# Performance work log

Measured on AMD Instinct MI355X. Metric: run time of the kernel, lower is better.

## Reference

```python
import jax, jax.numpy as jnp
import numpy as np
from jax import lax

B, T, Z, H, F = 64, 256, 128, 512, 64
EPS = 1e-3  # keras LayerNormalization default epsilon


def _glorot(key, shape):
    fan_in, fan_out = shape[0], shape[1]
    lim = np.sqrt(6.0 / (fan_in + fan_out)).astype(np.float32)
    return jax.random.uniform(key, shape, jnp.float32, -lim, lim)


def setup_inputs() -> dict:
    key = jax.random.key(0)
    ks = jax.random.split(key, 16)
    inp = {
        "z": jax.random.normal(ks[0], (B, T, Z), jnp.float32),
        "Wp": _glorot(ks[1], (Z, 2 * H)), "bp": jnp.zeros((2 * H,), jnp.float32),
        "Ws": _glorot(ks[2], (Z, H)), "bs": jnp.zeros((H,), jnp.float32),
        "K0": _glorot(ks[3], (2 * H, 4 * H)), "R0": _glorot(ks[4], (H, 4 * H)), "b0": jnp.zeros((4 * H,), jnp.float32),
        "K1": _glorot(ks[5], (H, 4 * H)), "R1": _glorot(ks[6], (H, 4 * H)), "b1": jnp.zeros((4 * H,), jnp.float32),
        "K2": _glorot(ks[7], (H, 4 * H)), "R2": _glorot(ks[8], (H, 4 * H)), "b2": jnp.zeros((4 * H,), jnp.float32),
        "gamma": jnp.ones((H,), jnp.float32), "beta": jnp.zeros((H,), jnp.float32),
        "W1": _glorot(ks[9], (H, H)), "b1d": jnp.zeros((H,), jnp.float32),
        "W2": _glorot(ks[10], (H, F)), "b2d": jnp.zeros((F,), jnp.float32),
    }
    return inp


def _lstm(x, K, R, b):
    # x: [B, T, D]; keras gate order i, f, g(c), o
    xK = jnp.swapaxes(jnp.einsum('btd,dg->btg', x, K) + b, 0, 1)  # [T, B, 4H]
    h0 = jnp.zeros((x.shape[0], H), x.dtype)
    c0 = jnp.zeros((x.shape[0], H), x.dtype)

    def step(carry, xk):
        h, c = carry
        zg = xk + h @ R
        i, f, g, o = jnp.split(zg, 4, axis=-1)
        c = jax.nn.sigmoid(f) * c + jax.nn.sigmoid(i) * jnp.tanh(g)
        h = jax.nn.sigmoid(o) * jnp.tanh(c)
        return (h, c), h

    _, hs = lax.scan(step, (h0, c0), xK)
    return jnp.swapaxes(hs, 0, 1)  # [B, T, H]


def reference(z, Wp, bp, Ws, bs, K0, R0, b0, K1, R1, b1, K2, R2, b2,
              gamma, beta, W1, b1d, W2, b2d):
    x = jnp.einsum('btz,zd->btd', z, Wp) + bp          # dense_proj -> [B,T,2H]
    residual = jnp.einsum('btz,zh->bth', z, Ws) + bs   # skip_proj  -> [B,T,H]
    x = _lstm(x, K0, R0, b0)
    x = _lstm(x, K1, R1, b1)
    x = x + residual  # use_residual, after layer index 1
    x = _lstm(x, K2, R2, b2)
    # training=False: dropout is identity and attention branch is skipped
    mu = jnp.mean(x, axis=-1, keepdims=True)
    var = jnp.mean(jnp.square(x - mu), axis=-1, keepdims=True)
    x = (x - mu) * lax.rsqrt(var + EPS) * gamma + beta
    x = jax.nn.relu(jnp.einsum('bth,hk->btk', x, W1) + b1d)
    x = jnp.tanh(jnp.einsum('bth,hf->btf', x, W2) + b2d)
    return x
```

## Files before the change

kernel.cpp:

```cpp
#include <hip/hip_runtime.h>
#include <hip/hip_fp16.h>
#include <stdint.h>

typedef unsigned short u16;
typedef unsigned int   u32;
typedef unsigned long long u64;
typedef __attribute__((ext_vector_type(8))) short s16x8;
typedef __attribute__((ext_vector_type(8))) _Float16 h16x8;
typedef __attribute__((ext_vector_type(4))) float f32x4;

#define T_LEN 256

__device__ __forceinline__ u16 f2h(float f){ return __half_as_ushort(__float2half(f)); }
__device__ __forceinline__ h16x8 as_h(s16x8 v){ union{s16x8 s; h16x8 h;} u; u.s=v; return u.h; }
__device__ __forceinline__ float sigm(float x){ return 1.f/(1.f + __expf(-x)); }
__device__ __forceinline__ float tanh_f(float x){ return 2.f*sigm(2.f*x) - 1.f; }

__device__ __forceinline__ s16x8 ldh(const u16* p){
  u64 lo = __hip_atomic_load((const u64*)p,       __ATOMIC_RELAXED, __HIP_MEMORY_SCOPE_AGENT);
  u64 hi = __hip_atomic_load((const u64*)(p + 4), __ATOMIC_RELAXED, __HIP_MEMORY_SCOPE_AGENT);
  union { u64 q[2]; s16x8 v; } u;
  u.q[0] = lo; u.q[1] = hi;
  return u.v;
}

__global__ void k_fuse(const float* __restrict__ Wp, const float* __restrict__ K0,
                       const float* __restrict__ Ws, const float* __restrict__ K2,
                       float* __restrict__ Wf0, float* __restrict__ Wf2)
{
  const int c  = blockIdx.x*256 + threadIdx.x;
  const int by = blockIdx.y;
  float acc[8] = {0,0,0,0,0,0,0,0};
  if (by < 16){
    const int r0 = by*8;
    for (int d = 0; d < 1024; ++d){
      float kv = K0[(size_t)d*2048 + c];
      #pragma unroll
      for (int ii = 0; ii < 8; ++ii) acc[ii] = fmaf(Wp[(size_t)(r0+ii)*1024 + d], kv, acc[ii]);
    }
    #pragma unroll
    for (int ii = 0; ii < 8; ++ii) Wf0[(size_t)(r0+ii)*2048 + c] = acc[ii];
  } else {
    const int r0 = (by-16)*8;
    for (int u = 0; u < 512; ++u){
      float kv = K2[(size_t)u*2048 + c];
      #pragma unroll
      for (int ii = 0; ii < 8; ++ii) acc[ii] = fmaf(Ws[(size_t)(r0+ii)*512 + u], kv, acc[ii]);
    }
    #pragma unroll
    for (int ii = 0; ii < 8; ++ii) Wf2[(size_t)(r0+ii)*2048 + c] = acc[ii];
  }
}

__global__ void k_bias(const float* __restrict__ bp, const float* __restrict__ K0,
                       const float* __restrict__ b0, const float* __restrict__ bs,
                       const float* __restrict__ K2, const float* __restrict__ b2,
                       float* __restrict__ gb0, float* __restrict__ gb2)
{
  const int bx = blockIdx.x;
  if (bx < 8){
    int c = bx*256 + threadIdx.x;
    float a = b0[c];
    for (int d = 0; d < 1024; ++d) a = fmaf(bp[d], K0[(size_t)d*2048 + c], a);
    gb0[c] = a;
  } else {
    int c = (bx-8)*256 + threadIdx.x;
    float a = b2[c];
    for (int u = 0; u < 512; ++u) a = fmaf(bs[u], K2[(size_t)u*2048 + c], a);
    gb2[c] = a;
  }
}

__global__ void k_zero(u32* __restrict__ hbz, int* __restrict__ done)
{
  int idx = blockIdx.x*256 + threadIdx.x;
  if (idx < 196608) hbz[idx] = 0u;
  if (blockIdx.x == 0 && threadIdx.x < 3) done[threadIdx.x*32] = 0;
}

__device__ __forceinline__ size_t gidx(int k, int c, int K32c){
  int gate = c >> 9, u = c & 511;
  int jj = u >> 3, uu = u & 7;
  int lc = gate*8 + uu;
  return ((size_t)(jj*2 + (lc>>4))*K32c + (k>>5))*512
         + (size_t)((((k>>3)&3)*16 + (lc&15))*8) + (size_t)(k&7);
}
__device__ __forceinline__ size_t fidx(int k, int c){
  return ((size_t)(c>>4)*16 + (k>>5))*512
         + (size_t)((((k>>3)&3)*16 + (c&15))*8) + (size_t)(k&7);
}

__global__ void k_pack(const float* __restrict__ R0, const float* __restrict__ Wf0,
                       const float* __restrict__ R1, const float* __restrict__ K1,
                       const float* __restrict__ R2, const float* __restrict__ K2,
                       const float* __restrict__ Wf2, const float* __restrict__ W1,
                       const float* __restrict__ W2, const float* __restrict__ z,
                       u16* __restrict__ wgt0, u16* __restrict__ wgt1, u16* __restrict__ wgt2,
                       u16* __restrict__ w1p,  u16* __restrict__ w2p,  u16* __restrict__ zp)
{
  const long NT = 8159232;
  for (long i = (long)blockIdx.x*256 + threadIdx.x; i < NT; i += (long)gridDim.x*256){
    if (i < 1310720){
      int k = (int)(i >> 11), c = (int)(i & 2047);
      float v = (k < 512) ? R0[(size_t)k*2048 + c] : Wf0[(size_t)(k-512)*2048 + c];
      wgt0[gidx(k, c, 20)] = f2h(v);
    } else if (i < 3407872){
      long i2 = i - 1310720; int k = (int)(i2 >> 11), c = (int)(i2 & 2047);
      float v = (k < 512) ? R1[(size_t)k*2048 + c] : K1[(size_t)(k-512)*2048 + c];
      wgt1[gidx(k, c, 32)] = f2h(v);
    } else if (i < 5767168){
      long i2 = i - 3407872; int k = (int)(i2 >> 11), c = (int)(i2 & 2047);
      float v = (k < 512)  ? R2[(size_t)k*2048 + c]
              : (k < 1024) ? K2[(size_t)(k-512)*2048 + c]
                           : Wf2[(size_t)(k-1024)*2048 + c];
      wgt2[gidx(k, c, 36)] = f2h(v);
    } else if (i < 6029312){
      long i2 = i - 5767168; int k = (int)(i2 >> 9), c = (int)(i2 & 511);
      w1p[fidx(k, c)] = f2h(W1[(size_t)k*512 + c]);
    } else if (i < 6062080){
      long i2 = i - 6029312; int k = (int)(i2 >> 6), c = (int)(i2 & 63);
      w2p[fidx(k, c)] = f2h(W2[(size_t)k*64 + c]);
    } else {
      long i2 = i - 6062080;
      int bb = (int)(i2 >> 15), rem = (int)(i2 & 32767);
      int tt = rem >> 7, k = rem & 127;
      zp[(((size_t)tt*4 + (bb>>4))*4 + (k>>5))*512
         + (size_t)((((k>>3)&3)*16 + (bb&15))*8) + (size_t)(k&7)] = f2h(z[i2]);
    }
  }
}

__global__ __launch_bounds__(256, 1) void k_wave(
    const u16* __restrict__ wgt0, const u16* __restrict__ wgt1, const u16* __restrict__ wgt2,
    const u16* __restrict__ zp, u16* __restrict__ hb, float* __restrict__ hout,
    int* done, u64* __restrict__ ackdump, const float* __restrict__ gb0,
    const float* __restrict__ b1g, const float* __restrict__ gb2)
{
  __shared__ __align__(16) u16 wsm[2*36*512];
  __shared__ float zg[64][33];
  __shared__ __align__(16) u16 hsh[64][8];
  const int tid = threadIdx.x;
  const int bid = blockIdx.x;
  const int L   = bid >> 6;
  const int j   = bid & 63;
  const int K32r = (L==0) ? 20 : ((L==1) ? 32 : 36);

  { const u16* wsrc = (L==0) ? wgt0 + (size_t)j*20480
                    : (L==1) ? wgt1 + (size_t)j*32768
                             : wgt2 + (size_t)j*36864;
    const uint4* s4 = (const uint4*)wsrc; uint4* d4 = (uint4*)wsm;
    const int n4 = K32r*128;
    for (int i = tid; i < n4; i += 256) d4[i] = s4[i]; }

  const int b    = tid & 63;
  const int q    = tid >> 6;
  const int w    = q;
  const int lane = tid & 63;

  float bias[2][4];
  { const float* bsrc = (L==0) ? gb0 : (L==1) ? b1g : gb2;
    #pragma unroll
    for (int ci = 0; ci < 2; ++ci){
      int ucol = j*8 + 2*q + ci;
      #pragma unroll
      for (int g = 0; g < 4; ++g) bias[ci][g] = bsrc[g*512 + ucol];
    } }
  float cst0 = 0.f, cst1 = 0.f;
  u64 ackacc = 0;

  const int smt   = tid >> 5;
  const int sbm   = (tid >> 1) & 15;
  const int shalf = tid & 1;
  const size_t schunk = ((size_t)(smt*16 + (j>>2))*64 + ((j&3)*16 + sbm))*8 + shalf*4;

  __syncthreads();

  for (int s = 0; s < T_LEN + 2; ++s){
    if (tid == 0){
      int g = 0;
      for (;;){
        int okk = 1;
        if (L > 0)
          okk &= (__hip_atomic_load(&done[(L-1)*32], __ATOMIC_RELAXED, __HIP_MEMORY_SCOPE_AGENT) >= 64*s);
        okk &= (__hip_atomic_load(&done[L*32],     __ATOMIC_RELAXED, __HIP_MEMORY_SCOPE_AGENT) >= 64*s);
        if (L < 2)
          okk &= (__hip_atomic_load(&done[(L+1)*32], __ATOMIC_RELAXED, __HIP_MEMORY_SCOPE_AGENT) >= 64*(s-2));
        if (okk || ++g > (1<<20)) break;
        __builtin_amdgcn_s_sleep(8);
      }
    }
    __syncthreads();

    const int t = s - L;
    float hv0 = 0.f, hv1 = 0.f;
    if (t >= 0 && t < T_LEN){
      const int slp = (s + 3) & 3;
      f32x4 acc0 = {0.f,0.f,0.f,0.f};
      f32x4 acc1 = {0.f,0.f,0.f,0.f};
      const size_t wl8 = (size_t)w*8192 + (size_t)lane*8;
      const u16* h0p = hb + (size_t)(0*4 + slp)*32768 + wl8;
      const u16* h1p = hb + (size_t)(1*4 + slp)*32768 + wl8;
      const u16* h2p = hb + (size_t)(2*4 + slp)*32768 + wl8;
      const u16* zpt = zp + (size_t)t*8192 + (size_t)w*2048 + (size_t)lane*8;

      if (L == 0){
        s16x8 areg[20];
        #pragma unroll
        for (int kk = 0; kk < 16; ++kk) areg[kk] = ldh(h0p + (size_t)kk*512);
        #pragma unroll
        for (int kk = 0; kk < 4; ++kk)  areg[16+kk] = *(const s16x8*)(zpt + (size_t)kk*512);
        #pragma unroll
        for (int kk = 0; kk < 20; ++kk){
          h16x8 bv0 = as_h(*(const s16x8*)&wsm[kk*512 + lane*8]);
          h16x8 bv1 = as_h(*(const s16x8*)&wsm[(20+kk)*512 + lane*8]);
          acc0 = __builtin_amdgcn_mfma_f32_16x16x32_f16(as_h(areg[kk]), bv0, acc0, 0, 0, 0);
          acc1 = __builtin_amdgcn_mfma_f32_16x16x32_f16(as_h(areg[kk]), bv1, acc1, 0, 0, 0);
        }
      } else if (L == 1){
        s16x8 areg[32];
        #pragma unroll
        for (int kk = 0; kk < 16; ++kk) areg[kk]    = ldh(h1p + (size_t)kk*512);
        #pragma unroll
        for (int kk = 0; kk < 16; ++kk) areg[16+kk] = ldh(h0p + (size_t)kk*512);
        #pragma unroll
        for (int kk = 0; kk < 32; ++kk){
          h16x8 bv0 = as_h(*(const s16x8*)&wsm[kk*512 + lane*8]);
          h16x8 bv1 = as_h(*(const s16x8*)&wsm[(32+kk)*512 + lane*8]);
          acc0 = __builtin_amdgcn_mfma_f32_16x16x32_f16(as_h(areg[kk]), bv0, acc0, 0, 0, 0);
          acc1 = __builtin_amdgcn_mfma_f32_16x16x32_f16(as_h(areg[kk]), bv1, acc1, 0, 0, 0);
        }
      } else {
        s16x8 areg[36];
        #pragma unroll
        for (int kk = 0; kk < 16; ++kk) areg[kk]    = ldh(h2p + (size_t)kk*512);
        #pragma unroll
        for (int kk = 0; kk < 16; ++kk) areg[16+kk] = ldh(h1p + (size_t)kk*512);
        #pragma unroll
        for (int kk = 0; kk < 4; ++kk)  areg[32+kk] = *(const s16x8*)(zpt + (size_t)kk*512);
        #pragma unroll
        for (int kk = 0; kk < 36; ++kk){
          h16x8 bv0 = as_h(*(const s16x8*)&wsm[kk*512 + lane*8]);
          h16x8 bv1 = as_h(*(const s16x8*)&wsm[(36+kk)*512 + lane*8]);
          acc0 = __builtin_amdgcn_mfma_f32_16x16x32_f16(as_h(areg[kk]), bv0, acc0, 0, 0, 0);
          acc1 = __builtin_amdgcn_mfma_f32_16x16x32_f16(as_h(areg[kk]), bv1, acc1, 0, 0, 0);
        }
      }
      #pragma unroll
      for (int r = 0; r < 4; ++r){
        int row = (w << 4) + ((lane >> 4) << 2) + r;
        zg[row][lane & 15]        = acc0[r];
        zg[row][16 + (lane & 15)] = acc1[r];
      }
      __syncthreads();

      {
        int uu = 2*q;
        float zi = zg[b][uu]      + bias[0][0];
        float zf = zg[b][8 + uu]  + bias[0][1];
        float zc = zg[b][16 + uu] + bias[0][2];
        float zo = zg[b][24 + uu] + bias[0][3];
        float cc = sigm(zf)*cst0 + sigm(zi)*tanh_f(zc);
        cst0 = cc; hv0 = sigm(zo)*tanh_f(cc);
      }
      {
        int uu = 2*q + 1;
        float zi = zg[b][uu]      + bias[1][0];
        float zf = zg[b][8 + uu]  + bias[1][1];
        float zc = zg[b][16 + uu] + bias[1][2];
        float zo = zg[b][24 + uu] + bias[1][3];
        float cc = sigm(zf)*cst1 + sigm(zi)*tanh_f(zc);
        cst1 = cc; hv1 = sigm(zo)*tanh_f(cc);
      }
      *(u32*)&hsh[b][2*q] = (u32)f2h(hv0) | ((u32)f2h(hv1) << 16);
      __syncthreads();
      if (tid < 128){
        u16* hdst = hb + (size_t)(L*4 + (s & 3))*32768;
        u64 v = *(const u64*)&hsh[smt*16 + sbm][shalf*4];
        u64 old = __hip_atomic_exchange((u64*)(hdst + schunk), v,
                                        __ATOMIC_RELAXED, __HIP_MEMORY_SCOPE_AGENT);
        ackacc ^= old;
      }
    }
    __syncthreads();
    if (tid == 0)
      __hip_atomic_fetch_add(&done[L*32], 1, __ATOMIC_RELAXED, __HIP_MEMORY_SCOPE_AGENT);
    if (L == 2 && t >= 0 && t < T_LEN){
      size_t o = ((size_t)t*64 + b)*512 + j*8 + 2*q;
      hout[o]     = hv0;
      hout[o + 1] = hv1;
    }
  }
  if (tid < 128) ackdump[((size_t)bid << 7) + tid] = ackacc;
}

__global__ __launch_bounds__(256) void k_ep(
    const float* __restrict__ hout, const float* __restrict__ gam, const float* __restrict__ bet,
    const u16* __restrict__ w1p, const u16* __restrict__ w2p,
    const float* __restrict__ b1d, const float* __restrict__ b2d, float* __restrict__ out)
{
  __shared__ __align__(16) u16 xf[32768];
  __shared__ __align__(16) u16 yf[32768];
  __shared__ float redS[64][8];
  __shared__ float muS[64], rsS[64];
  const int t = blockIdx.x, tid = threadIdx.x;
  const int r = tid >> 2, qq = tid & 3;

  const float4* x4 = (const float4*)(hout + ((size_t)t*64 + r)*512 + qq*128);
  float sum = 0.f, sq = 0.f;
  #pragma unroll 8
  for (int i = 0; i < 32; ++i){
    float4 v = x4[i];
    sum += v.x + v.y + v.z + v.w;
    sq  += v.x*v.x + v.y*v.y + v.z*v.z + v.w*v.w;
  }
  redS[r][qq] = sum; redS[r][4+qq] = sq;
  __syncthreads();
  if (qq == 0){
    float s1 = redS[r][0]+redS[r][1]+redS[r][2]+redS[r][3];
    float s2 = redS[r][4]+redS[r][5]+redS[r][6]+redS[r][7];
    float m  = s1 * (1.f/512.f);
    float var = s2 * (1.f/512.f) - m*m;
    muS[r] = m; rsS[r] = rsqrtf(var + 1e-3f);
  }
  __syncthreads();
  { const float m = muS[r], rstd = rsS[r];
    const int mt = r >> 4, rl = r & 15;
    for (int i = 0; i < 32; ++i){
      float4 v = x4[i];
      int k0 = qq*128 + i*4;
      float vv[4] = {v.x, v.y, v.z, v.w};
      #pragma unroll
      for (int e = 0; e < 4; ++e){
        int k = k0 + e;
        float xn = (vv[e] - m)*rstd*gam[k] + bet[k];
        xf[((mt*16 + (k>>5))*64 + ((k>>3)&3)*16 + rl)*8 + (k&7)] = f2h(xn);
      }
    } }
  __syncthreads();

  const int w = tid >> 6, lane = tid & 63;
  f32x4 acc[4][8];
  f32x4 vz = {0.f,0.f,0.f,0.f};
  #pragma unroll
  for (int a = 0; a < 4; ++a)
    #pragma unroll
    for (int n = 0; n < 8; ++n) acc[a][n] = vz;
  for (int k32 = 0; k32 < 16; ++k32){
    h16x8 av[4];
    #pragma unroll
    for (int mt = 0; mt < 4; ++mt) av[mt] = as_h(*(const s16x8*)&xf[((mt*16 + k32)*64 + lane)*8]);
    #pragma unroll
    for (int nn = 0; nn < 8; ++nn){
      const int n16 = w*8 + nn;
      h16x8 bv = as_h(*(const s16x8*)&w1p[((size_t)(n16*16 + k32)*64 + lane)*8]);
      #pragma unroll
      for (int mt = 0; mt < 4; ++mt)
        acc[mt][nn] = __builtin_amdgcn_mfma_f32_16x16x32_f16(av[mt], bv, acc[mt][nn], 0,0,0);
    }
  }
  #pragma unroll
  for (int nn = 0; nn < 8; ++nn){
    int col = (w*8 + nn)*16 + (lane & 15);
    float bv = b1d[col];
    #pragma unroll
    for (int mt = 0; mt < 4; ++mt){
      #pragma unroll
      for (int rr = 0; rr < 4; ++rr){
        int row = mt*16 + ((lane >> 4) << 2) + rr;
        float v = acc[mt][nn][rr] + bv;
        v = fmaxf(v, 0.f);
        yf[((mt*16 + (col>>5))*64 + ((col>>3)&3)*16 + (row&15))*8 + (col&7)] = f2h(v);
      } } }
  __syncthreads();

  f32x4 acc2[4];
  #pragma unroll
  for (int mt = 0; mt < 4; ++mt) acc2[mt] = vz;
  for (int k32 = 0; k32 < 16; ++k32){
    h16x8 bv = as_h(*(const s16x8*)&w2p[((size_t)(w*16 + k32)*64 + lane)*8]);
    #pragma unroll
    for (int mt = 0; mt < 4; ++mt){
      h16x8 av = as_h(*(const s16x8*)&yf[((mt*16 + k32)*64 + lane)*8]);
      acc2[mt] = __builtin_amdgcn_mfma_f32_16x16x32_f16(av, bv, acc2[mt], 0,0,0);
    } }
  const int f = w*16 + (lane & 15);
  const float bf_ = b2d[f];
  #pragma unroll
  for (int mt = 0; mt < 4; ++mt)
    #pragma unroll
    for (int rr = 0; rr < 4; ++rr){
      int row = mt*16 + ((lane >> 4) << 2) + rr;
      out[((size_t)row*T_LEN + t)*64 + f] = tanh_f(acc2[mt][rr] + bf_);
    }
}

extern "C" void kernel_launch(void* const* d_in, const int* in_sizes, int n_in,
                              void* d_out, int out_size, void* d_ws, size_t ws_size,
                              hipStream_t stream)
{
  const float* z    = (const float*)d_in[0];
  const float* Wp   = (const float*)d_in[1];
  const float* bp   = (const float*)d_in[2];
  const float* Ws   = (const float*)d_in[3];
  const float* bs   = (const float*)d_in[4];
  const float* K0   = (const float*)d_in[5];
  const float* R0   = (const float*)d_in[6];
  const float* b0   = (const float*)d_in[7];
  const float* K1   = (const float*)d_in[8];
  const float* R1   = (const float*)d_in[9];
  const float* b1   = (const float*)d_in[10];
  const float* K2   = (const float*)d_in[11];
  const float* R2   = (const float*)d_in[12];
  const float* b2   = (const float*)d_in[13];
  const float* gam  = (const float*)d_in[14];
  const float* bet  = (const float*)d_in[15];
  const float* W1   = (const float*)d_in[16];
  const float* b1d  = (const float*)d_in[17];
  const float* W2   = (const float*)d_in[18];
  const float* b2d  = (const float*)d_in[19];
  float* out = (float*)d_out;
  (void)in_sizes; (void)n_in; (void)out_size; (void)ws_size;

  char* base = (char*)d_ws;
  size_t off = 0;
  auto carve = [&](size_t bytes)->char* {
    char* p = base + off;
    off = (off + bytes + 255) & ~(size_t)255;
    return p;
  };
  u16*   wgt0 = (u16*)  carve((size_t)64*20480*2);
  u16*   wgt1 = (u16*)  carve((size_t)64*32768*2);
  u16*   wgt2 = (u16*)  carve((size_t)64*36864*2);
  u16*   w1p  = (u16*)  carve((size_t)262144*2);
  u16*   w2p  = (u16*)  carve((size_t)32768*2);
  u16*   zp   = (u16*)  carve((size_t)2097152*2);
  float* Wf0  = (float*)carve((size_t)262144*4);
  float* Wf2  = (float*)carve((size_t)262144*4);
  float* gb0  = (float*)carve((size_t)2048*4);
  float* gb2  = (float*)carve((size_t)2048*4);
  u16*   hb   = (u16*)  carve((size_t)393216*2);
  float* hout = (float*)carve((size_t)8388608*4);
  int*   done = (int*)  carve((size_t)512);
  u64*   ackd = (u64*)  carve((size_t)192*128*8);

  k_fuse<<<dim3(8,32), dim3(256), 0, stream>>>(Wp, K0, Ws, K2, Wf0, Wf2);
  k_bias<<<dim3(16),   dim3(256), 0, stream>>>(bp, K0, b0, bs, K2, b2, gb0, gb2);
  k_zero<<<dim3(768),  dim3(256), 0, stream>>>((u32*)hb, done);
  k_pack<<<dim3(4096), dim3(256), 0, stream>>>(R0, Wf0, R1, K1, R2, K2, Wf2, W1, W2, z,
                                               wgt0, wgt1, wgt2, w1p, w2p, zp);
  k_wave<<<dim3(192),  dim3(256), 0, stream>>>(wgt0, wgt1, wgt2, zp, hb, hout, done,
                                               ackd, gb0, b1, gb2);
  k_ep<<<dim3(256),    dim3(256), 0, stream>>>(hout, gam, bet, w1p, w2p, b1d, b2d, out);
}
```

Before: 2.076 ms.

## Replace ring hidden buffer and counter barrier with full-history buffer and per-block flags

The persistent wavefront LSTM kernel now stores every timestep's hidden state in a full per-layer history buffer instead of a 4-slot ring. The shared done counters become per-block step flags, polled by a whole wavefront with __all. That drops the back-pressure wait on the next layer and removes the need for atomic loads of h, which are now plain vector loads. The last layer no longer writes a separate fp32 hout array; the epilogue reads the fp16 history directly in MFMA layout and normalizes in place in shared memory. In exchange it uses more workspace, and LayerNorm now reads fp16 inputs, a small precision change. Plain loads of data written by other blocks also rely on the relaxed flag ordering being enough to make those writes visible.

```diff
diff --git a/kernel.cpp b/kernel.cpp
--- a/kernel.cpp
+++ b/kernel.cpp
@@ -12,17 +12,10 @@
 #define T_LEN 256
 
 __device__ __forceinline__ u16 f2h(float f){ return __half_as_ushort(__float2half(f)); }
+__device__ __forceinline__ float h2f(u16 x){ union{u16 u; _Float16 h;} c; c.u = x; return (float)c.h; }
 __device__ __forceinline__ h16x8 as_h(s16x8 v){ union{s16x8 s; h16x8 h;} u; u.s=v; return u.h; }
 __device__ __forceinline__ float sigm(float x){ return 1.f/(1.f + __expf(-x)); }
 __device__ __forceinline__ float tanh_f(float x){ return 2.f*sigm(2.f*x) - 1.f; }
-
-__device__ __forceinline__ s16x8 ldh(const u16* p){
-  u64 lo = __hip_atomic_load((const u64*)p,       __ATOMIC_RELAXED, __HIP_MEMORY_SCOPE_AGENT);
-  u64 hi = __hip_atomic_load((const u64*)(p + 4), __ATOMIC_RELAXED, __HIP_MEMORY_SCOPE_AGENT);
-  union { u64 q[2]; s16x8 v; } u;
-  u.q[0] = lo; u.q[1] = hi;
-  return u.v;
-}
 
 __global__ void k_fuse(const float* __restrict__ Wp, const float* __restrict__ K0,
                        const float* __restrict__ Ws, const float* __restrict__ K2,
@@ -71,11 +64,14 @@
   }
 }
 
-__global__ void k_zero(u32* __restrict__ hbz, int* __restrict__ done)
+__global__ void k_zero(u32* __restrict__ hfz, int* __restrict__ flags)
 {
   int idx = blockIdx.x*256 + threadIdx.x;
-  if (idx < 196608) hbz[idx] = 0u;
-  if (blockIdx.x == 0 && threadIdx.x < 3) done[threadIdx.x*32] = 0;
+  if (idx < 49152){
+    int L = idx >> 14, off = idx & 16383;
+    hfz[(size_t)L*257*16384 + off] = 0u;
+  }
+  if (blockIdx.x == 0 && threadIdx.x < 192) flags[threadIdx.x] = -1;
 }
 
 __device__ __forceinline__ size_t gidx(int k, int c, int K32c){
@@ -132,8 +128,8 @@
 
 __global__ __launch_bounds__(256, 1) void k_wave(
     const u16* __restrict__ wgt0, const u16* __restrict__ wgt1, const u16* __restrict__ wgt2,
-    const u16* __restrict__ zp, u16* __restrict__ hb, float* __restrict__ hout,
-    int* done, u64* __restrict__ ackdump, const float* __restrict__ gb0,
+    const u16* __restrict__ zp, u16* __restrict__ hf, int* flags,
+    u64* __restrict__ ackdump, const float* __restrict__ gb0,
     const float* __restrict__ b1g, const float* __restrict__ gb2)
 {
   __shared__ __align__(16) u16 wsm[2*36*512];
@@ -176,39 +172,36 @@
   __syncthreads();
 
   for (int s = 0; s < T_LEN + 2; ++s){
-    if (tid == 0){
+    if (q == 0){
+      const int need = s - 1;
       int g = 0;
       for (;;){
-        int okk = 1;
+        int okk = (__hip_atomic_load(&flags[L*64 + lane], __ATOMIC_RELAXED,
+                                     __HIP_MEMORY_SCOPE_AGENT) >= need);
         if (L > 0)
-          okk &= (__hip_atomic_load(&done[(L-1)*32], __ATOMIC_RELAXED, __HIP_MEMORY_SCOPE_AGENT) >= 64*s);
-        okk &= (__hip_atomic_load(&done[L*32],     __ATOMIC_RELAXED, __HIP_MEMORY_SCOPE_AGENT) >= 64*s);
-        if (L < 2)
-          okk &= (__hip_atomic_load(&done[(L+1)*32], __ATOMIC_RELAXED, __HIP_MEMORY_SCOPE_AGENT) >= 64*(s-2));
-        if (okk || ++g > (1<<20)) break;
-        __builtin_amdgcn_s_sleep(8);
+          okk &= (__hip_atomic_load(&flags[(L-1)*64 + lane], __ATOMIC_RELAXED,
+                                    __HIP_MEMORY_SCOPE_AGENT) >= need);
+        if (__all(okk) || ++g > (1<<20)) break;
+        __builtin_amdgcn_s_sleep(2);
       }
     }
     __syncthreads();
 
     const int t = s - L;
-    float hv0 = 0.f, hv1 = 0.f;
     if (t >= 0 && t < T_LEN){
-      const int slp = (s + 3) & 3;
       f32x4 acc0 = {0.f,0.f,0.f,0.f};
       f32x4 acc1 = {0.f,0.f,0.f,0.f};
       const size_t wl8 = (size_t)w*8192 + (size_t)lane*8;
-      const u16* h0p = hb + (size_t)(0*4 + slp)*32768 + wl8;
-      const u16* h1p = hb + (size_t)(1*4 + slp)*32768 + wl8;
-      const u16* h2p = hb + (size_t)(2*4 + slp)*32768 + wl8;
-      const u16* zpt = zp + (size_t)t*8192 + (size_t)w*2048 + (size_t)lane*8;
+      const u16* hself = hf + ((size_t)(L*257 + t))*32768 + wl8;
+      const u16* hblw  = (L > 0) ? hf + ((size_t)((L-1)*257 + t + 1))*32768 + wl8 : nullptr;
+      const u16* zpt   = zp + (size_t)t*8192 + (size_t)w*2048 + (size_t)lane*8;
 
       if (L == 0){
         s16x8 areg[20];
         #pragma unroll
-        for (int kk = 0; kk < 16; ++kk) areg[kk] = ldh(h0p + (size_t)kk*512);
-        #pragma unroll
-        for (int kk = 0; kk < 4; ++kk)  areg[16+kk] = *(const s16x8*)(zpt + (size_t)kk*512);
+        for (int kk = 0; kk < 16; ++kk) areg[kk]    = *(const s16x8*)(hself + (size_t)kk*512);
+        #pragma unroll
+        for (int kk = 0; kk < 4; ++kk)  areg[16+kk] = *(const s16x8*)(zpt   + (size_t)kk*512);
         #pragma unroll
         for (int kk = 0; kk < 20; ++kk){
           h16x8 bv0 = as_h(*(const s16x8*)&wsm[kk*512 + lane*8]);
@@ -219,9 +212,9 @@
       } else if (L == 1){
         s16x8 areg[32];
         #pragma unroll
-        for (int kk = 0; kk < 16; ++kk) areg[kk]    = ldh(h1p + (size_t)kk*512);
-        #pragma unroll
-        for (int kk = 0; kk < 16; ++kk) areg[16+kk] = ldh(h0p + (size_t)kk*512);
+        for (int kk = 0; kk < 16; ++kk) areg[kk]    = *(const s16x8*)(hself + (size_t)kk*512);
+        #pragma unroll
+        for (int kk = 0; kk < 16; ++kk) areg[16+kk] = *(const s16x8*)(hblw  + (size_t)kk*512);
         #pragma unroll
         for (int kk = 0; kk < 32; ++kk){
           h16x8 bv0 = as_h(*(const s16x8*)&wsm[kk*512 + lane*8]);
@@ -232,11 +225,11 @@
       } else {
         s16x8 areg[36];
         #pragma unroll
-        for (int kk = 0; kk < 16; ++kk) areg[kk]    = ldh(h2p + (size_t)kk*512);
-        #pragma unroll
-        for (int kk = 0; kk < 16; ++kk) areg[16+kk] = ldh(h1p + (size_t)kk*512);
-        #pragma unroll
-        for (int kk = 0; kk < 4; ++kk)  areg[32+kk] = *(const s16x8*)(zpt + (size_t)kk*512);
+        for (int kk = 0; kk < 16; ++kk) areg[kk]    = *(const s16x8*)(hself + (size_t)kk*512);
+        #pragma unroll
+        for (int kk = 0; kk < 16; ++kk) areg[16+kk] = *(const s16x8*)(hblw  + (size_t)kk*512);
+        #pragma unroll
+        for (int kk = 0; kk < 4; ++kk)  areg[32+kk] = *(const s16x8*)(zpt   + (size_t)kk*512);
         #pragma unroll
         for (int kk = 0; kk < 36; ++kk){
           h16x8 bv0 = as_h(*(const s16x8*)&wsm[kk*512 + lane*8]);
@@ -253,6 +246,7 @@
       }
       __syncthreads();
 
+      float hv0, hv1;
       {
         int uu = 2*q;
         float zi = zg[b][uu]      + bias[0][0];
@@ -274,7 +268,7 @@
       *(u32*)&hsh[b][2*q] = (u32)f2h(hv0) | ((u32)f2h(hv1) << 16);
       __syncthreads();
       if (tid < 128){
-        u16* hdst = hb + (size_t)(L*4 + (s & 3))*32768;
+        u16* hdst = hf + ((size_t)(L*257 + t + 1))*32768;
         u64 v = *(const u64*)&hsh[smt*16 + sbm][shalf*4];
         u64 old = __hip_atomic_exchange((u64*)(hdst + schunk), v,
                                         __ATOMIC_RELAXED, __HIP_MEMORY_SCOPE_AGENT);
@@ -283,36 +277,42 @@
     }
     __syncthreads();
     if (tid == 0)
-      __hip_atomic_fetch_add(&done[L*32], 1, __ATOMIC_RELAXED, __HIP_MEMORY_SCOPE_AGENT);
-    if (L == 2 && t >= 0 && t < T_LEN){
-      size_t o = ((size_t)t*64 + b)*512 + j*8 + 2*q;
-      hout[o]     = hv0;
-      hout[o + 1] = hv1;
-    }
+      __hip_atomic_store(&flags[L*64 + j], s, __ATOMIC_RELAXED, __HIP_MEMORY_SCOPE_AGENT);
   }
   if (tid < 128) ackdump[((size_t)bid << 7) + tid] = ackacc;
 }
 
 __global__ __launch_bounds__(256) void k_ep(
-    const float* __restrict__ hout, const float* __restrict__ gam, const float* __restrict__ bet,
+    const u16* __restrict__ hf, const float* __restrict__ gam, const float* __restrict__ bet,
     const u16* __restrict__ w1p, const u16* __restrict__ w2p,
     const float* __restrict__ b1d, const float* __restrict__ b2d, float* __restrict__ out)
 {
-  __shared__ __align__(16) u16 xf[32768];
+  __shared__ __align__(16) u16 xs[32768];
   __shared__ __align__(16) u16 yf[32768];
   __shared__ float redS[64][8];
   __shared__ float muS[64], rsS[64];
   const int t = blockIdx.x, tid = threadIdx.x;
+
+  { const uint4* src = (const uint4*)(hf + ((size_t)(2*257 + t + 1))*32768);
+    uint4* dst = (uint4*)xs;
+    #pragma unroll
+    for (int i = 0; i < 16; ++i) dst[tid + 256*i] = src[tid + 256*i]; }
+  __syncthreads();
+
   const int r = tid >> 2, qq = tid & 3;
-
-  const float4* x4 = (const float4*)(hout + ((size_t)t*64 + r)*512 + qq*128);
+  const int mt = r >> 4, ml = r & 15;
   float sum = 0.f, sq = 0.f;
-  #pragma unroll 8
-  for (int i = 0; i < 32; ++i){
-    float4 v = x4[i];
-    sum += v.x + v.y + v.z + v.w;
-    sq  += v.x*v.x + v.y*v.y + v.z*v.z + v.w*v.w;
-  }
+  #pragma unroll
+  for (int k32 = qq*4; k32 < qq*4 + 4; ++k32)
+    #pragma unroll
+    for (int kq = 0; kq < 4; ++kq){
+      s16x8 v = *(const s16x8*)&xs[(((mt*16 + k32)*64) + kq*16 + ml)*8];
+      #pragma unroll
+      for (int e = 0; e < 8; ++e){
+        float x = h2f(((const u16*)&v)[e]);
+        sum += x; sq += x*x;
+      }
+    }
   redS[r][qq] = sum; redS[r][4+qq] = sq;
   __syncthreads();
   if (qq == 0){
@@ -324,18 +324,19 @@
   }
   __syncthreads();
   { const float m = muS[r], rstd = rsS[r];
-    const int mt = r >> 4, rl = r & 15;
-    for (int i = 0; i < 32; ++i){
-      float4 v = x4[i];
-      int k0 = qq*128 + i*4;
-      float vv[4] = {v.x, v.y, v.z, v.w};
-      #pragma unroll
-      for (int e = 0; e < 4; ++e){
-        int k = k0 + e;
-        float xn = (vv[e] - m)*rstd*gam[k] + bet[k];
-        xf[((mt*16 + (k>>5))*64 + ((k>>3)&3)*16 + rl)*8 + (k&7)] = f2h(xn);
-      }
-    } }
+    #pragma unroll
+    for (int k32 = qq*4; k32 < qq*4 + 4; ++k32)
+      #pragma unroll
+      for (int kq = 0; kq < 4; ++kq){
+        u16* pp = &xs[(((mt*16 + k32)*64) + kq*16 + ml)*8];
+        s16x8 v = *(const s16x8*)pp;
+        #pragma unroll
+        for (int e = 0; e < 8; ++e){
+          int k = k32*32 + kq*8 + e;
+          float xn = (h2f(((const u16*)&v)[e]) - m)*rstd*gam[k] + bet[k];
+          pp[e] = f2h(xn);
+        }
+      } }
   __syncthreads();
 
   const int w = tid >> 6, lane = tid & 63;
@@ -348,14 +349,14 @@
   for (int k32 = 0; k32 < 16; ++k32){
     h16x8 av[4];
     #pragma unroll
-    for (int mt = 0; mt < 4; ++mt) av[mt] = as_h(*(const s16x8*)&xf[((mt*16 + k32)*64 + lane)*8]);
+    for (int mt2 = 0; mt2 < 4; ++mt2) av[mt2] = as_h(*(const s16x8*)&xs[((mt2*16 + k32)*64 + lane)*8]);
     #pragma unroll
     for (int nn = 0; nn < 8; ++nn){
       const int n16 = w*8 + nn;
       h16x8 bv = as_h(*(const s16x8*)&w1p[((size_t)(n16*16 + k32)*64 + lane)*8]);
       #pragma unroll
-      for (int mt = 0; mt < 4; ++mt)
-        acc[mt][nn] = __builtin_amdgcn_mfma_f32_16x16x32_f16(av[mt], bv, acc[mt][nn], 0,0,0);
+      for (int mt2 = 0; mt2 < 4; ++mt2)
+        acc[mt2][nn] = __builtin_amdgcn_mfma_f32_16x16x32_f16(av[mt2], bv, acc[mt2][nn], 0,0,0);
     }
   }
   #pragma unroll
@@ -363,34 +364,34 @@
     int col = (w*8 + nn)*16 + (lane & 15);
     float bv = b1d[col];
     #pragma unroll
-    for (int mt = 0; mt < 4; ++mt){
+    for (int mt2 = 0; mt2 < 4; ++mt2){
       #pragma unroll
       for (int rr = 0; rr < 4; ++rr){
-        int row = mt*16 + ((lane >> 4) << 2) + rr;
-        float v = acc[mt][nn][rr] + bv;
+        int row = mt2*16 + ((lane >> 4) << 2) + rr;
+        float v = acc[mt2][nn][rr] + bv;
         v = fmaxf(v, 0.f);
-        yf[((mt*16 + (col>>5))*64 + ((col>>3)&3)*16 + (row&15))*8 + (col&7)] = f2h(v);
+        yf[((mt2*16 + (col>>5))*64 + ((col>>3)&3)*16 + (row&15))*8 + (col&7)] = f2h(v);
       } } }
   __syncthreads();
 
   f32x4 acc2[4];
   #pragma unroll
-  for (int mt = 0; mt < 4; ++mt) acc2[mt] = vz;
+  for (int mt2 = 0; mt2 < 4; ++mt2) acc2[mt2] = vz;
   for (int k32 = 0; k32 < 16; ++k32){
     h16x8 bv = as_h(*(const s16x8*)&w2p[((size_t)(w*16 + k32)*64 + lane)*8]);
     #pragma unroll
-    for (int mt = 0; mt < 4; ++mt){
-      h16x8 av = as_h(*(const s16x8*)&yf[((mt*16 + k32)*64 + lane)*8]);
-      acc2[mt] = __builtin_amdgcn_mfma_f32_16x16x32_f16(av, bv, acc2[mt], 0,0,0);
+    for (int mt2 = 0; mt2 < 4; ++mt2){
+      h16x8 av = as_h(*(const s16x8*)&yf[((mt2*16 + k32)*64 + lane)*8]);
+      acc2[mt2] = __builtin_amdgcn_mfma_f32_16x16x32_f16(av, bv, acc2[mt2], 0,0,0);
     } }
   const int f = w*16 + (lane & 15);
   const float bf_ = b2d[f];
   #pragma unroll
-  for (int mt = 0; mt < 4; ++mt)
+  for (int mt2 = 0; mt2 < 4; ++mt2)
     #pragma unroll
     for (int rr = 0; rr < 4; ++rr){
-      int row = mt*16 + ((lane >> 4) << 2) + rr;
-      out[((size_t)row*T_LEN + t)*64 + f] = tanh_f(acc2[mt][rr] + bf_);
+      int row = mt2*16 + ((lane >> 4) << 2) + rr;
+      out[((size_t)row*T_LEN + t)*64 + f] = tanh_f(acc2[mt2][rr] + bf_);
     }
 }
 
@@ -438,17 +439,16 @@
   float* Wf2  = (float*)carve((size_t)262144*4);
   float* gb0  = (float*)carve((size_t)2048*4);
   float* gb2  = (float*)carve((size_t)2048*4);
-  u16*   hb   = (u16*)  carve((size_t)393216*2);
-  float* hout = (float*)carve((size_t)8388608*4);
-  int*   done = (int*)  carve((size_t)512);
+  u16*   hf   = (u16*)  carve((size_t)3*257*32768*2);
+  int*   flags= (int*)  carve((size_t)1024);
   u64*   ackd = (u64*)  carve((size_t)192*128*8);
 
   k_fuse<<<dim3(8,32), dim3(256), 0, stream>>>(Wp, K0, Ws, K2, Wf0, Wf2);
   k_bias<<<dim3(16),   dim3(256), 0, stream>>>(bp, K0, b0, bs, K2, b2, gb0, gb2);
-  k_zero<<<dim3(768),  dim3(256), 0, stream>>>((u32*)hb, done);
+  k_zero<<<dim3(768),  dim3(256), 0, stream>>>((u32*)hf, flags);
   k_pack<<<dim3(4096), dim3(256), 0, stream>>>(R0, Wf0, R1, K1, R2, K2, Wf2, W1, W2, z,
                                                wgt0, wgt1, wgt2, w1p, w2p, zp);
-  k_wave<<<dim3(192),  dim3(256), 0, stream>>>(wgt0, wgt1, wgt2, zp, hb, hout, done,
+  k_wave<<<dim3(192),  dim3(256), 0, stream>>>(wgt0, wgt1, wgt2, zp, hf, flags,
                                                ackd, gb0, b1, gb2);
-  k_ep<<<dim3(256),    dim3(256), 0, stream>>>(hout, gam, bet, w1p, w2p, b1d, b2d, out);
-}
+  k_ep<<<dim3(256),    dim3(256), 0, stream>>>(hf, gam, bet, w1p, w2p, b1d, b2d, out);
+}
```

Result: faster. 1.930 ms (-7.0%).
